# Kernel tuning notes

Measured on AMD Instinct MI355X. Metric: run time of the kernel, lower is better.

Reference implementation:

```python
import jax, jax.numpy as jnp
import numpy as np

ALPHA = 0.2          # LeakyReLU negative slope
NEG_INF = -9e15      # standard GAT masking constant


def gat_layer(h, adj_mask, W, a_src, a_dst):
    # h: [N, D], adj_mask: [N, N] bool
    Wh = h @ W                                  # [N, D]
    e = (Wh @ a_src)[:, None] + (Wh @ a_dst)[None, :]  # [N, N]
    e = jax.nn.leaky_relu(e, negative_slope=ALPHA)
    e = jnp.where(adj_mask, e, NEG_INF)
    attn = jax.nn.softmax(e, axis=-1)           # [N, N]
    return jax.nn.relu(attn @ Wh)               # PlainGCN applies ReLU


def setup_inputs() -> dict:
    key = jax.random.key(0)
    ks = jax.random.split(key, 8)
    N, D = 8192, 256
    x = jax.random.normal(ks[0], (N, D), dtype=jnp.float32)
    adj = jax.random.randint(ks[1], (N, N), 0, 2, dtype=jnp.int32)
    s = 1.0 / np.sqrt(D)
    W1 = jax.random.normal(ks[2], (D, D), dtype=jnp.float32) * s
    a1_src = jax.random.normal(ks[3], (D,), dtype=jnp.float32) * s
    a1_dst = jax.random.normal(ks[4], (D,), dtype=jnp.float32) * s
    W2 = jax.random.normal(ks[5], (D, D), dtype=jnp.float32) * s
    a2_src = jax.random.normal(ks[6], (D,), dtype=jnp.float32) * s
    a2_dst = jax.random.normal(ks[7], (D,), dtype=jnp.float32) * s
    return {"x": x, "adj": adj, "W1": W1, "a1_src": a1_src, "a1_dst": a1_dst,
            "W2": W2, "a2_src": a2_src, "a2_dst": a2_dst}


def reference(x, adj, W1, a1_src, a1_dst, W2, a2_src, a2_dst):
    adj_mask = adj > 0
    h = gat_layer(x, adj_mask, W1, a1_src, a1_dst)
    h = gat_layer(h, adj_mask, W2, a2_src, a2_dst)
    return h
```

## Files before the change

kernel.cpp:

```cpp
#include <hip/hip_runtime.h>
#include <cstdint>
#include <cstddef>


#define ALPHA 0.2f
#define NN 8192
#define DD 256

typedef __attribute__((ext_vector_type(8))) short short8;
typedef __attribute__((ext_vector_type(4))) float f32x4;

__device__ __forceinline__ unsigned bf16rne(float x) {
    union { float f; unsigned u; } c; c.f = x;
    return (c.u + 0x7fffu + ((c.u >> 16) & 1u)) >> 16;
}

#if __has_builtin(__builtin_amdgcn_cvt_pk_bf16_f32)
__device__ __forceinline__ unsigned pk_bf16(float a, float b) {
    return __builtin_bit_cast(unsigned, __builtin_amdgcn_cvt_pk_bf16_f32(a, b));
}
#else
__device__ __forceinline__ unsigned pk_bf16(float a, float b) {
    return bf16rne(a) | (bf16rne(b) << 16);
}
#endif


__device__ __forceinline__ void packbits_dev(const int* __restrict__ adj,
                                             uint64_t* __restrict__ bits,
                                             int row, int lane) {
    const int* rowp = adj + (size_t)row * NN;
    uint64_t* dst = bits + (size_t)row * 128;
    for (int it = 0; it < 16; it++) {
        const int* p = rowp + it * 512;
        int a0 = p[lane];
        int a1 = p[64 + lane];
        int a2 = p[128 + lane];
        int a3 = p[192 + lane];
        int a4 = p[256 + lane];
        int a5 = p[320 + lane];
        int a6 = p[384 + lane];
        int a7 = p[448 + lane];
        uint64_t m0 = __ballot(a0 != 0);
        uint64_t m1 = __ballot(a1 != 0);
        uint64_t m2 = __ballot(a2 != 0);
        uint64_t m3 = __ballot(a3 != 0);
        uint64_t m4 = __ballot(a4 != 0);
        uint64_t m5 = __ballot(a5 != 0);
        uint64_t m6 = __ballot(a6 != 0);
        uint64_t m7 = __ballot(a7 != 0);
        if (lane == 0) {
            dst[it * 8 + 0] = m0; dst[it * 8 + 1] = m1;
            dst[it * 8 + 2] = m2; dst[it * 8 + 3] = m3;
            dst[it * 8 + 4] = m4; dst[it * 8 + 5] = m5;
            dst[it * 8 + 6] = m6; dst[it * 8 + 7] = m7;
        }
    }
}

__device__ __forceinline__ void transp_dev(const uint32_t* __restrict__ bits32,
                                           uint32_t* __restrict__ bitsT,
                                           int job, unsigned char* smem, int t) {
    uint32_t (*tile)[65] = (uint32_t (*)[65])smem;
    const int i0 = (job >> 2) * 64;
    const int w0 = (job & 3) * 64;
#pragma unroll
    for (int p = 0; p < 4; p++) {
        int r = (t >> 4) + 16 * p;
        int c4 = (t & 15) * 4;
        uint4 v = *(const uint4*)(bits32 + (size_t)(i0 + r) * 256 + w0 + c4);
        tile[r][c4 + 0] = v.x; tile[r][c4 + 1] = v.y;
        tile[r][c4 + 2] = v.z; tile[r][c4 + 3] = v.w;
    }
    __syncthreads();
#pragma unroll
    for (int p = 0; p < 4; p++) {
        int wr = (t >> 4) + 16 * p;
        int i4 = (t & 15) * 4;
        uint4 o = {tile[i4][wr], tile[i4 + 1][wr], tile[i4 + 2][wr], tile[i4 + 3][wr]};
        *(uint4*)(bitsT + (size_t)(w0 + wr) * NN + i0 + i4) = o;
    }
}

__device__ __forceinline__ void gemm_dev(const float* __restrict__ A,
                                         const float* __restrict__ B,
                                         unsigned short* __restrict__ Bpack,
                                         const float* __restrict__ a_src,
                                         const float* __restrict__ a_dst,
                                         float* __restrict__ s4,
                                         float* __restrict__ dd4,
                                         int job, unsigned char* smem, int t) {
    float (*At)[36] = (float (*)[36])smem;
    float2 (*Bs)[32] = (float2 (*)[32])(smem + 4608);
    const int m0 = (job >> 2) * 32;
    const int cq = job & 3;
    const int r0 = (t >> 5) * 4;
    const int cl = t & 31;
    float acc[4][2];
#pragma unroll
    for (int i = 0; i < 4; i++) { acc[i][0] = 0.f; acc[i][1] = 0.f; }

    for (int k0 = 0; k0 < DD; k0 += 32) {
        {
            int row = t >> 3, kq = t & 7;
            float4 v = *(const float4*)(A + (size_t)(m0 + row) * DD + k0 + kq * 4);
            At[kq * 4 + 0][row] = v.x; At[kq * 4 + 1][row] = v.y;
            At[kq * 4 + 2][row] = v.z; At[kq * 4 + 3][row] = v.w;
        }
#pragma unroll
        for (int l2 = 0; l2 < 2; l2++) {
            int fi = l2 * 256 + t;
            int br = fi >> 4, bc4 = fi & 15;
            float4 v = *(const float4*)(B + (size_t)(k0 + br) * DD + cq * 64 + bc4 * 4);
            Bs[br][bc4 * 2] = {v.x, v.y};
            Bs[br][bc4 * 2 + 1] = {v.z, v.w};
        }
        __syncthreads();
#pragma unroll
        for (int k = 0; k < 32; k++) {
            float4 a0 = *(const float4*)&At[k][r0];
            float2 b = Bs[k][cl];
            float av[4] = {a0.x, a0.y, a0.z, a0.w};
#pragma unroll
            for (int i = 0; i < 4; i++) {
                acc[i][0] += av[i] * b.x;
                acc[i][1] += av[i] * b.y;
            }
        }
        __syncthreads();
    }

    const int jt = m0 >> 5;
    const int lq = ((r0 >> 3) & 3) * 16;
    const int i8 = r0 & 4;
#pragma unroll
    for (int cc = 0; cc < 2; cc++) {
        int c = cq * 64 + cl * 2 + cc;
        int ct = c >> 4;
        int lane = lq + (c & 15);
        uint2 pk;
        pk.x = pk_bf16(acc[0][cc], acc[1][cc]);
        pk.y = pk_bf16(acc[2][cc], acc[3][cc]);
        *(uint2*)(Bpack + ((size_t)(jt * 16 + ct) * 64 + lane) * 8 + i8) = pk;
    }

    const int c0 = cq * 64 + cl * 2;
    float as0 = a_src[c0], as1 = a_src[c0 + 1];
    float ad0 = a_dst[c0], ad1 = a_dst[c0 + 1];
    float ps[4], pd[4];
#pragma unroll
    for (int i = 0; i < 4; i++) {
        ps[i] = acc[i][0] * as0 + acc[i][1] * as1;
        pd[i] = acc[i][0] * ad0 + acc[i][1] * ad1;
    }
#pragma unroll
    for (int off = 16; off; off >>= 1) {
#pragma unroll
        for (int i = 0; i < 4; i++) {
            ps[i] += __shfl_xor(ps[i], off);
            pd[i] += __shfl_xor(pd[i], off);
        }
    }
    if (cl == 0) {
#pragma unroll
        for (int i = 0; i < 4; i++) {
            s4[(size_t)cq * NN + m0 + r0 + i] = ps[i];
            dd4[(size_t)cq * NN + m0 + r0 + i] = pd[i];
        }
    }
}

__device__ __forceinline__ void rowstats_dev(const uint32_t* __restrict__ bits32,
                                             const float* __restrict__ s,
                                             const float* __restrict__ dd,
                                             const float* __restrict__ FH,
                                             float* __restrict__ Ep,
                                             float* __restrict__ Gp,
                                             int job, unsigned char* smem, int t) {
    uint32_t* smk = (uint32_t*)smem;
    float (*red)[4] = (float (*)[4])(smem + 4096);
    float* sEm = (float*)(smem + 4096 + 64);
    float* sEa = (float*)(smem + 4096 + 80);
    const int i0 = job * 4;
    const int wave = t >> 6, lane = t & 63;
    {
        const uint4* src = (const uint4*)(bits32 + (size_t)i0 * 256);
        ((uint4*)smk)[t] = src[t];
    }
    __syncthreads();

    float mx[4];
#pragma unroll
    for (int r = 0; r < 4; r++) mx[r] = -3.0e38f;
#pragma unroll
    for (int q = 0; q < 8; q++) {
        float4 v = *(const float4*)(dd + 4 * (t + 256 * q));
        const int wq = 32 * q + (t >> 3);
        const int sh = (t & 7) * 4;
#pragma unroll
        for (int r = 0; r < 4; r++) {
            uint32_t b = smk[r * 256 + wq] >> sh;
            mx[r] = fmaxf(mx[r], (b & 1u) ? v.x : -3.0e38f);
            mx[r] = fmaxf(mx[r], (b & 2u) ? v.y : -3.0e38f);
            mx[r] = fmaxf(mx[r], (b & 4u) ? v.z : -3.0e38f);
            mx[r] = fmaxf(mx[r], (b & 8u) ? v.w : -3.0e38f);
        }
    }
#pragma unroll
    for (int r = 0; r < 4; r++) {
#pragma unroll
        for (int off = 32; off; off >>= 1) mx[r] = fmaxf(mx[r], __shfl_down(mx[r], off));
    }
    if (lane == 0) {
#pragma unroll
        for (int r = 0; r < 4; r++) red[wave][r] = mx[r];
    }
    __syncthreads();
    if (t < 4) {
        float dmax = fmaxf(fmaxf(red[0][t], red[1][t]), fmaxf(red[2][t], red[3][t]));
        float si = s[i0 + t];
        float e = si + dmax;
        float m = e >= 0.f ? e : ALPHA * e;
        sEm[t] = __expf(si - m);
        sEa[t] = __expf(ALPHA * si - m);
    }
    __syncthreads();
    float em[4], ea[4], sm[4];
#pragma unroll
    for (int r = 0; r < 4; r++) { em[r] = sEm[r]; ea[r] = sEa[r]; sm[r] = 0.f; }

#pragma unroll
    for (int q = 0; q < 16; q++) {
        float4 v = *(const float4*)(FH + 4 * (t + 256 * q));
        const int wq = 16 * q + (t >> 4);
        const int sh = (t & 15) * 2;
#pragma unroll
        for (int r = 0; r < 4; r++) {
            uint32_t b = smk[r * 256 + wq] >> sh;
            float c0 = fmaxf(em[r] * v.x, ea[r] * v.y);
            float c1 = fmaxf(em[r] * v.z, ea[r] * v.w);
            sm[r] += (b & 1u) ? c0 : 0.f;
            sm[r] += (b & 2u) ? c1 : 0.f;
        }
    }
#pragma unroll
    for (int r = 0; r < 4; r++) {
#pragma unroll
        for (int off = 32; off; off >>= 1) sm[r] += __shfl_down(sm[r], off);
    }
    __syncthreads();
    if (lane == 0) {
#pragma unroll
        for (int r = 0; r < 4; r++) red[wave][r] = sm[r];
    }
    __syncthreads();
    if (t < 4) {
        float rl = 1.0f / (red[0][t] + red[1][t] + red[2][t] + red[3][t]);
        Ep[i0 + t] = rl * sEm[t];
        Gp[i0 + t] = rl * sEa[t];
    }
}


__global__ __launch_bounds__(256) void mega1(const float* __restrict__ A,
                                             const float* __restrict__ W,
                                             unsigned short* __restrict__ Bpack,
                                             const float* __restrict__ a_src,
                                             const float* __restrict__ a_dst,
                                             float* __restrict__ s4,
                                             float* __restrict__ dd4,
                                             const int* __restrict__ adj,
                                             uint64_t* __restrict__ bits) {
    __shared__ __align__(16) unsigned char smem[12800];
    const int bx = blockIdx.x;
    const int t = threadIdx.x;
    const int sel = bx % 3;
    const int base = bx / 3;
    if (sel == 0) {
        gemm_dev(A, W, Bpack, a_src, a_dst, s4, dd4, base, smem, t);
    } else {
        const int row = base * 8 + (sel - 1) * 4 + (t >> 6);
        packbits_dev(adj, bits, row, t & 63);
    }
}

__global__ __launch_bounds__(256) void mega2(const uint32_t* __restrict__ bits32,
                                             uint32_t* __restrict__ bitsT,
                                             const float* __restrict__ s,
                                             const float* __restrict__ dd,
                                             const float* __restrict__ FH,
                                             float* __restrict__ Ep,
                                             float* __restrict__ Gp) {
    __shared__ __align__(16) unsigned char smem[16640];
    const int bx = blockIdx.x;
    const int t = threadIdx.x;
    const int sel = bx % 5;
    const int base = bx / 5;
    if (sel == 0) {
        transp_dev(bits32, bitsT, base, smem, t);
    } else {
        rowstats_dev(bits32, s, dd, FH, Ep, Gp, base * 4 + (sel - 1), smem, t);
    }
}

__global__ __launch_bounds__(256) void k_gemm(const float* A, const float* W,
                                              unsigned short* Bpack,
                                              const float* a_src, const float* a_dst,
                                              float* s4, float* dd4) {
    __shared__ __align__(16) unsigned char smem[12800];
    gemm_dev(A, W, Bpack, a_src, a_dst, s4, dd4, blockIdx.x, smem, threadIdx.x);
}
__global__ __launch_bounds__(256) void k_rowstats(const uint32_t* bits32, const float* s,
                                                  const float* dd, const float* FH,
                                                  float* Ep, float* Gp) {
    __shared__ __align__(16) unsigned char smem[4200];
    rowstats_dev(bits32, s, dd, FH, Ep, Gp, blockIdx.x, smem, threadIdx.x);
}

__global__ __launch_bounds__(256) void fhgen(const float* __restrict__ s4,
                                             const float* __restrict__ dd4,
                                             float* __restrict__ s,
                                             float* __restrict__ dd,
                                             float* __restrict__ FH) {
    int i = blockIdx.x * 256 + threadIdx.x;
    float ssum = (s4[i] + s4[i + NN]) + (s4[i + 2 * NN] + s4[i + 3 * NN]);
    float dsum = (dd4[i] + dd4[i + NN]) + (dd4[i + 2 * NN] + dd4[i + 3 * NN]);
    s[i] = ssum;
    dd[i] = dsum;
    FH[2 * i] = __expf(dsum);
    FH[2 * i + 1] = __expf(ALPHA * dsum);
}

__global__ __launch_bounds__(256, 4) void pv_mfma(const unsigned short* __restrict__ Bpack,
                                                  const uint32_t* __restrict__ bitsT,
                                                  const float* __restrict__ FH,
                                                  const float* __restrict__ Ep,
                                                  const float* __restrict__ Gp,
                                                  float* __restrict__ pout) {
    const int t = threadIdx.x;
    const int w = t >> 6, l = t & 63;
    const int bx = blockIdx.x;
    const int ks = bx & 7;
    const int cg = (bx >> 3) & 3;
    const int i0 = (bx >> 5) * 256 + w * 64;
    const int kbase = ks * 32;

    const int rl16 = l & 15;
    const int ko = (l >> 4) * 8;
    const int r0 = i0 + rl16;
    float Epv[4], Gpv[4];
#pragma unroll
    for (int f = 0; f < 4; f++) {
        Epv[f] = Ep[r0 + 16 * f];
        Gpv[f] = Gp[r0 + 16 * f];
    }

    const unsigned short* bb = Bpack + ((size_t)(cg * 4) * 64 + l) * 8;
    const uint32_t* btb = bitsT + i0 + rl16;

    f32x4 acc[4][4];
#pragma unroll
    for (int i = 0; i < 4; i++)
#pragma unroll
        for (int q = 0; q < 4; q++) acc[i][q] = (f32x4){0.f, 0.f, 0.f, 0.f};

    for (int jl = 0; jl < 32; jl++) {
        const int cc = kbase + jl;
        const unsigned short* bp = bb + (size_t)cc * 8192;
        short8 B0 = *(const short8*)(bp);
        short8 B1 = *(const short8*)(bp + 512);
        short8 B2 = *(const short8*)(bp + 1024);
        short8 B3 = *(const short8*)(bp + 1536);
        const uint32_t* btc = btb + (size_t)cc * NN;
        uint32_t bw0 = btc[0];
        uint32_t bw1 = btc[16];
        uint32_t bw2 = btc[32];
        uint32_t bw3 = btc[48];
        const float* fp = FH + 2 * (size_t)(cc * 32 + ko);
        float4 f0 = *(const float4*)(fp);
        float4 f1 = *(const float4*)(fp + 4);
        float4 f2 = *(const float4*)(fp + 8);
        float4 f3 = *(const float4*)(fp + 12);

        uint32_t bwa[4] = {bw0, bw1, bw2, bw3};
#pragma unroll
        for (int f = 0; f < 4; f++) {
            uint32_t wl = bwa[f] >> ko;
            float Epf = Epv[f], Gpf = Gpv[f];
            float p0 = (wl & 1u)   ? fmaxf(Epf * f0.x, Gpf * f0.y) : 0.f;
            float p1 = (wl & 2u)   ? fmaxf(Epf * f0.z, Gpf * f0.w) : 0.f;
            float p2 = (wl & 4u)   ? fmaxf(Epf * f1.x, Gpf * f1.y) : 0.f;
            float p3 = (wl & 8u)   ? fmaxf(Epf * f1.z, Gpf * f1.w) : 0.f;
            float p4 = (wl & 16u)  ? fmaxf(Epf * f2.x, Gpf * f2.y) : 0.f;
            float p5 = (wl & 32u)  ? fmaxf(Epf * f2.z, Gpf * f2.w) : 0.f;
            float p6 = (wl & 64u)  ? fmaxf(Epf * f3.x, Gpf * f3.y) : 0.f;
            float p7 = (wl & 128u) ? fmaxf(Epf * f3.z, Gpf * f3.w) : 0.f;
            uint4 au = {pk_bf16(p0, p1), pk_bf16(p2, p3), pk_bf16(p4, p5), pk_bf16(p6, p7)};
            short8 af = __builtin_bit_cast(short8, au);
            acc[f][0] = __builtin_amdgcn_mfma_f32_16x16x32_bf16(af, B0, acc[f][0], 0, 0, 0);
            acc[f][1] = __builtin_amdgcn_mfma_f32_16x16x32_bf16(af, B1, acc[f][1], 0, 0, 0);
            acc[f][2] = __builtin_amdgcn_mfma_f32_16x16x32_bf16(af, B2, acc[f][2], 0, 0, 0);
            acc[f][3] = __builtin_amdgcn_mfma_f32_16x16x32_bf16(af, B3, acc[f][3], 0, 0, 0);
        }
    }

    float* outp = pout + (size_t)ks * NN * DD;
#pragma unroll
    for (int f = 0; f < 4; f++) {
        const int orow = i0 + 16 * f + (l >> 4) * 4;
#pragma unroll
        for (int q = 0; q < 4; q++) {
            const int ocol = cg * 64 + q * 16 + rl16;
#pragma unroll
            for (int r = 0; r < 4; r++)
                outp[(size_t)(orow + r) * DD + ocol] = acc[f][q][r];
        }
    }
}

__global__ __launch_bounds__(256) void combine8(const float* __restrict__ p,
                                                float* __restrict__ out) {
    const size_t S = (size_t)NN * DD / 4;
    size_t idx = (size_t)blockIdx.x * 256 + threadIdx.x;
    float4 a0 = ((const float4*)p)[idx];
    float4 a1 = ((const float4*)p)[idx + S];
    float4 a2 = ((const float4*)p)[idx + 2 * S];
    float4 a3 = ((const float4*)p)[idx + 3 * S];
    float4 a4 = ((const float4*)p)[idx + 4 * S];
    float4 a5 = ((const float4*)p)[idx + 5 * S];
    float4 a6 = ((const float4*)p)[idx + 6 * S];
    float4 a7 = ((const float4*)p)[idx + 7 * S];
    float4 o;
    o.x = fmaxf(((a0.x + a1.x) + (a2.x + a3.x)) + ((a4.x + a5.x) + (a6.x + a7.x)), 0.f);
    o.y = fmaxf(((a0.y + a1.y) + (a2.y + a3.y)) + ((a4.y + a5.y) + (a6.y + a7.y)), 0.f);
    o.z = fmaxf(((a0.z + a1.z) + (a2.z + a3.z)) + ((a4.z + a5.z) + (a6.z + a7.z)), 0.f);
    o.w = fmaxf(((a0.w + a1.w) + (a2.w + a3.w)) + ((a4.w + a5.w) + (a6.w + a7.w)), 0.f);
    ((float4*)out)[idx] = o;
}

extern "C" void kernel_launch(void* const* d_in, const int* in_sizes, int n_in,
                              void* d_out, int out_size, void* d_ws, size_t ws_size,
                              hipStream_t stream) {
    const float* x   = (const float*)d_in[0];
    const int* adj   = (const int*)d_in[1];
    const float* W1  = (const float*)d_in[2];
    const float* a1s = (const float*)d_in[3];
    const float* a1d = (const float*)d_in[4];
    const float* W2  = (const float*)d_in[5];
    const float* a2s = (const float*)d_in[6];
    const float* a2d = (const float*)d_in[7];
    float* out = (float*)d_out;

    char* ws = (char*)d_ws;
    const size_t MB = 1024ull * 1024ull;
    uint64_t*       bits  = (uint64_t*)(ws + 8 * MB);
    uint32_t*       bits32= (uint32_t*)bits;
    uint32_t*       bitsT = (uint32_t*)(ws + 16 * MB);
    float*          sArr  = (float*)(ws + 24 * MB);
    float*          ddA   = sArr + NN;
    float*          EpA   = sArr + 2 * NN;
    float*          GpA   = sArr + 3 * NN;
    float*          FHA   = sArr + 4 * NN;
    float*          s4    = sArr + 6 * NN;
    float*          dd4   = sArr + 10 * NN;
    unsigned short* Bpack = (unsigned short*)(ws + 25 * MB);
    float*          pout  = (float*)(ws + 32 * MB);

    mega1<<<dim3(3072), dim3(256), 0, stream>>>(x, W1, Bpack, a1s, a1d, s4, dd4,
                                                adj, bits);
    fhgen<<<dim3(32), dim3(256), 0, stream>>>(s4, dd4, sArr, ddA, FHA);
    mega2<<<dim3(2560), dim3(256), 0, stream>>>(bits32, bitsT, sArr, ddA, FHA, EpA, GpA);
    pv_mfma<<<dim3(1024), dim3(256), 0, stream>>>(Bpack, bitsT, FHA, EpA, GpA, pout);
    combine8<<<dim3(2048), dim3(256), 0, stream>>>(pout, out);

    k_gemm<<<dim3(1024), dim3(256), 0, stream>>>(out, W2, Bpack, a2s, a2d, s4, dd4);
    fhgen<<<dim3(32), dim3(256), 0, stream>>>(s4, dd4, sArr, ddA, FHA);
    k_rowstats<<<dim3(2048), dim3(256), 0, stream>>>(bits32, sArr, ddA, FHA, EpA, GpA);
    pv_mfma<<<dim3(1024), dim3(256), 0, stream>>>(Bpack, bitsT, FHA, EpA, GpA, pout);
    combine8<<<dim3(2048), dim3(256), 0, stream>>>(pout, out);
}
```

Baseline: 642.1 us.

## Share computed attention tiles across waves via LDS instead of recomputing per column group

Each block now covers 64 rows and all 256 output columns. Every wave computes the masked exp attention weights for its own 16 rows once and publishes them to double-buffered shared memory, and the other waves read them back for their column group. Before, each 64-row tile of weights was recomputed by four blocks, one per column group. This removes that 4x redundant exp/mask/convert work and the extra bit-mask and factor loads. The cost is a __syncthreads per k-step, LDS traffic, and a grid with the same block count but a different block-to-data mapping.

After: 588.9 us. 8.3% less time.

```diff
diff --git a/kernel.cpp b/kernel.cpp
--- a/kernel.cpp
+++ b/kernel.cpp
@@ -337,26 +337,22 @@
                                                   const float* __restrict__ Ep,
                                                   const float* __restrict__ Gp,
                                                   float* __restrict__ pout) {
+    __shared__ __align__(16) short8 pb[2][256];
     const int t = threadIdx.x;
     const int w = t >> 6, l = t & 63;
     const int bx = blockIdx.x;
     const int ks = bx & 7;
-    const int cg = (bx >> 3) & 3;
-    const int i0 = (bx >> 5) * 256 + w * 64;
+    const int i0 = (bx >> 3) * 64;
     const int kbase = ks * 32;
 
     const int rl16 = l & 15;
     const int ko = (l >> 4) * 8;
-    const int r0 = i0 + rl16;
-    float Epv[4], Gpv[4];
-#pragma unroll
-    for (int f = 0; f < 4; f++) {
-        Epv[f] = Ep[r0 + 16 * f];
-        Gpv[f] = Gp[r0 + 16 * f];
-    }
-
-    const unsigned short* bb = Bpack + ((size_t)(cg * 4) * 64 + l) * 8;
-    const uint32_t* btb = bitsT + i0 + rl16;
+    const int rw = i0 + 16 * w + rl16;
+    const float Epw = Ep[rw];
+    const float Gpw = Gp[rw];
+
+    const unsigned short* bb = Bpack + ((size_t)(w * 4) * 64 + l) * 8;
+    const uint32_t* btb = bitsT + rw;
 
     f32x4 acc[4][4];
 #pragma unroll
@@ -366,37 +362,39 @@
 
     for (int jl = 0; jl < 32; jl++) {
         const int cc = kbase + jl;
+        const int par = jl & 1;
         const unsigned short* bp = bb + (size_t)cc * 8192;
         short8 B0 = *(const short8*)(bp);
         short8 B1 = *(const short8*)(bp + 512);
         short8 B2 = *(const short8*)(bp + 1024);
         short8 B3 = *(const short8*)(bp + 1536);
-        const uint32_t* btc = btb + (size_t)cc * NN;
-        uint32_t bw0 = btc[0];
-        uint32_t bw1 = btc[16];
-        uint32_t bw2 = btc[32];
-        uint32_t bw3 = btc[48];
+        uint32_t bw = btb[(size_t)cc * NN];
         const float* fp = FH + 2 * (size_t)(cc * 32 + ko);
         float4 f0 = *(const float4*)(fp);
         float4 f1 = *(const float4*)(fp + 4);
         float4 f2 = *(const float4*)(fp + 8);
         float4 f3 = *(const float4*)(fp + 12);
 
-        uint32_t bwa[4] = {bw0, bw1, bw2, bw3};
+        uint32_t wl = bw >> ko;
+        float p0 = (wl & 1u)   ? fmaxf(Epw * f0.x, Gpw * f0.y) : 0.f;
+        float p1 = (wl & 2u)   ? fmaxf(Epw * f0.z, Gpw * f0.w) : 0.f;
+        float p2 = (wl & 4u)   ? fmaxf(Epw * f1.x, Gpw * f1.y) : 0.f;
+        float p3 = (wl & 8u)   ? fmaxf(Epw * f1.z, Gpw * f1.w) : 0.f;
+        float p4 = (wl & 16u)  ? fmaxf(Epw * f2.x, Gpw * f2.y) : 0.f;
+        float p5 = (wl & 32u)  ? fmaxf(Epw * f2.z, Gpw * f2.w) : 0.f;
+        float p6 = (wl & 64u)  ? fmaxf(Epw * f3.x, Gpw * f3.y) : 0.f;
+        float p7 = (wl & 128u) ? fmaxf(Epw * f3.z, Gpw * f3.w) : 0.f;
+        uint4 au = {pk_bf16(p0, p1), pk_bf16(p2, p3), pk_bf16(p4, p5), pk_bf16(p6, p7)};
+        short8 aown = __builtin_bit_cast(short8, au);
+        pb[par][w * 64 + l] = aown;
+
+        __syncthreads();
+
 #pragma unroll
         for (int f = 0; f < 4; f++) {
-            uint32_t wl = bwa[f] >> ko;
-            float Epf = Epv[f], Gpf = Gpv[f];
-            float p0 = (wl & 1u)   ? fmaxf(Epf * f0.x, Gpf * f0.y) : 0.f;
-            float p1 = (wl & 2u)   ? fmaxf(Epf * f0.z, Gpf * f0.w) : 0.f;
-            float p2 = (wl & 4u)   ? fmaxf(Epf * f1.x, Gpf * f1.y) : 0.f;
-            float p3 = (wl & 8u)   ? fmaxf(Epf * f1.z, Gpf * f1.w) : 0.f;
-            float p4 = (wl & 16u)  ? fmaxf(Epf * f2.x, Gpf * f2.y) : 0.f;
-            float p5 = (wl & 32u)  ? fmaxf(Epf * f2.z, Gpf * f2.w) : 0.f;
-            float p6 = (wl & 64u)  ? fmaxf(Epf * f3.x, Gpf * f3.y) : 0.f;
-            float p7 = (wl & 128u) ? fmaxf(Epf * f3.z, Gpf * f3.w) : 0.f;
-            uint4 au = {pk_bf16(p0, p1), pk_bf16(p2, p3), pk_bf16(p4, p5), pk_bf16(p6, p7)};
-            short8 af = __builtin_bit_cast(short8, au);
+            short8 af;
+            if (f == w) af = aown;
+            else        af = pb[par][f * 64 + l];
             acc[f][0] = __builtin_amdgcn_mfma_f32_16x16x32_bf16(af, B0, acc[f][0], 0, 0, 0);
             acc[f][1] = __builtin_amdgcn_mfma_f32_16x16x32_bf16(af, B1, acc[f][1], 0, 0, 0);
             acc[f][2] = __builtin_amdgcn_mfma_f32_16x16x32_bf16(af, B2, acc[f][2], 0, 0, 0);
@@ -410,7 +408,7 @@
         const int orow = i0 + 16 * f + (l >> 4) * 4;
 #pragma unroll
         for (int q = 0; q < 4; q++) {
-            const int ocol = cg * 64 + q * 16 + rl16;
+            const int ocol = w * 64 + q * 16 + rl16;
 #pragma unroll
             for (int r = 0; r < 4; r++)
                 outp[(size_t)(orow + r) * DD + ocol] = acc[f][q][r];
```
